# Performance work log

Measured on AMD Instinct MI355X. Metric: run time of the kernel, lower is better.

The kernel has to match this reference:

```python
import jax, jax.numpy as jnp
import numpy as np

N = 400_000      # active sparse voxels
C = 128          # hidden_size
GRID = 128       # dense grid extent per axis
KVOL = 27        # 3x3x3 kernel offsets


def _build_kmap():
    """Build a consistent neighbor map (the 'kmap') from random sparse voxel coords."""
    rng = np.random.default_rng(0)
    lin = np.sort(rng.choice(GRID ** 3, size=N, replace=False).astype(np.int64))
    lookup = np.full(GRID ** 3, -1, dtype=np.int32)
    lookup[lin] = np.arange(N, dtype=np.int32)
    x = lin // (GRID * GRID)
    y = (lin // GRID) % GRID
    z = lin % GRID
    nbr = np.full((N, KVOL), -1, dtype=np.int32)
    k = 0
    for dx in (-1, 0, 1):
        for dy in (-1, 0, 1):
            for dz in (-1, 0, 1):
                nx, ny, nz = x + dx, y + dy, z + dz
                valid = (nx >= 0) & (nx < GRID) & (ny >= 0) & (ny < GRID) & \
                        (nz >= 0) & (nz < GRID)
                nlin = (nx * GRID + ny) * GRID + nz
                nbr[:, k] = np.where(valid, lookup[np.clip(nlin, 0, GRID ** 3 - 1)], -1)
                k += 1
    return nbr


def setup_inputs() -> dict:
    key = jax.random.key(0)
    ks = jax.random.split(key, 6)
    s = 1.0 / np.sqrt(C)
    return {
        "feats": jax.random.normal(ks[0], (N, C), jnp.float32),
        "neighbor_idx": jnp.asarray(_build_kmap()),
        "conv_w": jax.random.normal(ks[1], (KVOL, C, C), jnp.float32) * (s / np.sqrt(KVOL)),
        "conv_b": jax.random.normal(ks[2], (C,), jnp.float32) * 0.01,
        "lin_w": jax.random.normal(ks[3], (C, C), jnp.float32) * s,   # torch Linear weight [out,in]
        "lin_b": jax.random.normal(ks[4], (C,), jnp.float32) * 0.01,
        "ln_g": jnp.ones((C,), jnp.float32),
        "ln_b": jnp.zeros((C,), jnp.float32),
    }


def reference(feats, neighbor_idx, conv_w, conv_b, lin_w, lin_b, ln_g, ln_b):
    # --- sparse 3x3x3 conv via kmap gather-GEMM-accumulate ---
    out = jnp.zeros_like(feats)
    for k in range(KVOL):  # fixed small structural loop over kernel offsets
        idx = neighbor_idx[:, k]
        valid = (idx >= 0)[:, None]
        gathered = jnp.where(valid, feats[jnp.maximum(idx, 0)], 0.0)  # [N, C]
        out = out + gathered @ conv_w[k]
    out = out + conv_b                      # conv bias add on jagged data
    # --- Linear (torch: x @ W.T + b) ---
    out = out @ lin_w.T + lin_b
    # --- LayerNorm over channel dim (eps=1e-5) ---
    mu = jnp.mean(out, axis=-1, keepdims=True)
    var = jnp.mean(jnp.square(out - mu), axis=-1, keepdims=True)
    out = (out - mu) * jax.lax.rsqrt(var + 1e-5) * ln_g + ln_b
    return out
```

## Files before the change

### kernel.cpp

```cpp
#include <hip/hip_runtime.h>

typedef __bf16 bf16;
typedef unsigned short u16;
typedef __attribute__((ext_vector_type(8))) __bf16 bf16x8;
typedef __attribute__((ext_vector_type(4))) float f32x4;
typedef const __attribute__((address_space(1))) char gchar;

#define N_PTS 400000
#define KVOL 27
#define SCHED0() __builtin_amdgcn_sched_barrier(0)

__device__ __forceinline__ f32x4 mfma16(bf16x8 a, bf16x8 b, f32x4 c) {
  return __builtin_amdgcn_mfma_f32_16x16x32_bf16(a, b, c, 0, 0, 0);
}

__global__ __launch_bounds__(256) void cast_feats_k(const float4* __restrict__ in,
                                                    bf16x8* __restrict__ out) {
  int i = blockIdx.x * 256 + threadIdx.x;
  float4 a = in[2 * i], b = in[2 * i + 1];
  bf16x8 v;
  v[0] = (bf16)a.x; v[1] = (bf16)a.y; v[2] = (bf16)a.z; v[3] = (bf16)a.w;
  v[4] = (bf16)b.x; v[5] = (bf16)b.y; v[6] = (bf16)b.z; v[7] = (bf16)b.w;
  out[i] = v;
}

__global__ __launch_bounds__(256) void cast_w_k(const float* __restrict__ conv_w,
                                                const float* __restrict__ lin_w,
                                                bf16x8* __restrict__ wt,
                                                bf16x8* __restrict__ lt,
                                                bf16x8* __restrict__ zrow) {
  int t = blockIdx.x * 256 + threadIdx.x;
  if (t < KVOL * 128 * 16) {
    int k = t >> 11;
    int rem = t & 2047;
    int co = rem >> 4;
    int cp = rem & 15;
    int cl = cp ^ (co & 7);
    bf16x8 v;
#pragma unroll
    for (int j = 0; j < 8; ++j) {
      int ci = cl * 8 + j;
      v[j] = (bf16)conv_w[(k * 128 + ci) * 128 + co];
    }
    wt[t] = v;
  } else if (t < KVOL * 128 * 16 + 2048) {
    int t2 = t - KVOL * 128 * 16;
    bf16x8 v;
#pragma unroll
    for (int j = 0; j < 8; ++j) v[j] = (bf16)lin_w[t2 * 8 + j];
    lt[t2] = v;
  } else if (t < KVOL * 128 * 16 + 2048 + 16) {
    bf16x8 v = {};
    zrow[t - (KVOL * 128 * 16 + 2048)] = v;
  }
}

__global__ __launch_bounds__(256, 2) void fused_k(
    const bf16* __restrict__ featsb,
    const int* __restrict__ nbr,
    const bf16* __restrict__ wt,
    const bf16* __restrict__ lt,
    const bf16* __restrict__ zrow,
    const float* __restrict__ conv_b,
    const float* __restrict__ lin_b,
    const float* __restrict__ ln_g,
    const float* __restrict__ ln_b,
    float* __restrict__ out) {
  __shared__ __align__(16) u16 wdb[2][16384];

  const int tid = threadIdx.x;
  const int lane = tid & 63;
  const int wv = tid >> 6;
  const int l15 = lane & 15;
  const int l4 = lane >> 4;
  const int lp = lane & 7;

  const int nwg = gridDim.x;
  const int bid0 = blockIdx.x;
  const int q = nwg >> 3, r8 = nwg & 7;
  const int xcd = bid0 & 7, lo = bid0 >> 3;
  const int bid = (xcd < r8 ? xcd * (q + 1) : r8 * (q + 1) + (xcd - r8) * q) + lo;

  const int row0 = bid * 256;
  const int rb = row0 + wv * 64 + l15;
  const int aoff = l4 * 16;

  {
    const char* g = (const char*)wt + (size_t)tid * 16;
    char* l = (char*)(&wdb[0][0]) + wv * 1024;
#pragma unroll
    for (int c = 0; c < 8; ++c)
      __builtin_amdgcn_global_load_lds(
          (const __attribute__((address_space(1))) void*)(g + c * 4096),
          (__attribute__((address_space(3))) void*)(l + c * 4096), 16, 0, 0);
  }
  int idx_nxt[4];
  int idx_t0[4];
#pragma unroll
  for (int rg = 0; rg < 4; ++rg) {
    int r = rb + rg * 16;
    int rr = r < N_PTS ? r : N_PTS - 1;
    int v0 = nbr[(size_t)rr * KVOL + 0];
    int v1 = nbr[(size_t)rr * KVOL + 1];
    idx_t0[rg] = r < N_PTS ? v0 : -1;
    idx_nxt[rg] = r < N_PTS ? v1 : -1;
  }
  bf16x8 a[4][4];
#pragma unroll
  for (int rg = 0; rg < 4; ++rg) {
    gchar* base = (idx_t0[rg] < 0)
                      ? (gchar*)zrow
                      : (gchar*)featsb + (size_t)idx_t0[rg] * 256;
    base += aoff;
#pragma unroll
    for (int kf = 0; kf < 4; ++kf) a[rg][kf] = *(const __attribute__((address_space(1))) bf16x8*)(base + kf * 64);
  }
  f32x4 acc[4][8];
#pragma unroll
  for (int rg = 0; rg < 4; ++rg)
#pragma unroll
    for (int ct = 0; ct < 8; ++ct) acc[rg][ct] = (f32x4)0.f;

  SCHED0();
  asm volatile("s_waitcnt vmcnt(0)" ::: "memory");
  SCHED0();
  __builtin_amdgcn_s_barrier();
  SCHED0();

  int cur = 0;
  for (int t = 0; t < KVOL; ++t) {
    {
      int tn = t + 1 < KVOL ? t + 1 : KVOL - 1;
      const char* g = (const char*)wt + (size_t)tn * 32768 + (size_t)tid * 16;
      char* l = (char*)(&wdb[cur ^ 1][0]) + wv * 1024;
#pragma unroll
      for (int c = 0; c < 8; ++c)
        __builtin_amdgcn_global_load_lds(
            (const __attribute__((address_space(1))) void*)(g + c * 4096),
            (__attribute__((address_space(3))) void*)(l + c * 4096), 16, 0, 0);
    }
    gchar* nb[4];
#pragma unroll
    for (int rg = 0; rg < 4; ++rg) {
      gchar* base = (idx_nxt[rg] < 0)
                        ? (gchar*)zrow
                        : (gchar*)featsb + (size_t)idx_nxt[rg] * 256;
      nb[rg] = base + aoff;
    }
    {
      int k2 = t + 2 < KVOL ? t + 2 : KVOL - 1;
#pragma unroll
      for (int rg = 0; rg < 4; ++rg) {
        int r = rb + rg * 16;
        int rr = r < N_PTS ? r : N_PTS - 1;
        int v = nbr[(size_t)rr * KVOL + k2];
        idx_nxt[rg] = r < N_PTS ? v : -1;
      }
    }
    SCHED0();
    asm volatile("s_waitcnt vmcnt(32)" ::: "memory");
    SCHED0();
    __builtin_amdgcn_s_barrier();
    SCHED0();
    const u16* wb = &wdb[cur][0];
#pragma unroll
    for (int kf = 0; kf < 4; ++kf) {
      const int chunk = (kf * 4 + l4) ^ lp;
      const u16* bp = wb + l15 * 128 + chunk * 8;
#pragma unroll
      for (int ct = 0; ct < 8; ++ct) {
        bf16x8 b = *(const bf16x8*)(bp + ct * 2048);
#pragma unroll
        for (int rg = 0; rg < 4; ++rg)
          acc[rg][ct] = mfma16(a[rg][kf], b, acc[rg][ct]);
      }
#pragma unroll
      for (int rg = 0; rg < 4; ++rg)
        a[rg][kf] = *(const __attribute__((address_space(1))) bf16x8*)(nb[rg] + kf * 64);
    }
    SCHED0();
    __builtin_amdgcn_s_barrier();
    SCHED0();
    cur ^= 1;
  }

  SCHED0();
  asm volatile("s_waitcnt vmcnt(0)" ::: "memory");
  SCHED0();
  __builtin_amdgcn_s_barrier();
  SCHED0();

  u16* cobuf = &wdb[0][0];
  float cb[8];
#pragma unroll
  for (int ct = 0; ct < 8; ++ct) cb[ct] = conv_b[ct * 16 + l15];
#pragma unroll
  for (int rg = 0; rg < 4; ++rg) {
#pragma unroll
    for (int ct = 0; ct < 8; ++ct) {
#pragma unroll
      for (int j = 0; j < 4; ++j) {
        int rl = wv * 64 + rg * 16 + l4 * 4 + j;
        int c = ct * 16 + l15;
        float x = acc[rg][ct][j] + cb[ct];
        int chunk = (c >> 3) ^ (rl & 7);
        cobuf[rl * 128 + chunk * 8 + (c & 7)] = __builtin_bit_cast(u16, (bf16)x);
      }
    }
  }
  SCHED0();
  asm volatile("s_waitcnt lgkmcnt(0)" ::: "memory");
  SCHED0();
  __builtin_amdgcn_s_barrier();
  SCHED0();

  f32x4 acc2[4][8];
#pragma unroll
  for (int rg = 0; rg < 4; ++rg)
#pragma unroll
    for (int ct = 0; ct < 8; ++ct) acc2[rg][ct] = (f32x4)0.f;
#pragma unroll
  for (int kf = 0; kf < 4; ++kf) {
    const int chunk = (kf * 4 + l4) ^ lp;
    bf16x8 av[4];
#pragma unroll
    for (int rg = 0; rg < 4; ++rg)
      av[rg] = *(const bf16x8*)(cobuf + (wv * 64 + rg * 16 + l15) * 128 + chunk * 8);
#pragma unroll
    for (int ct = 0; ct < 8; ++ct) {
      bf16x8 b = *(const bf16x8*)(lt + (ct * 16 + l15) * 128 + (kf * 4 + l4) * 8);
#pragma unroll
      for (int rg = 0; rg < 4; ++rg)
        acc2[rg][ct] = mfma16(av[rg], b, acc2[rg][ct]);
    }
  }

  float lb[8], lg[8], lbv[8];
#pragma unroll
  for (int ct = 0; ct < 8; ++ct) {
    int c = ct * 16 + l15;
    lb[ct] = lin_b[c]; lg[ct] = ln_g[c]; lbv[ct] = ln_b[c];
  }
#pragma unroll
  for (int rg = 0; rg < 4; ++rg) {
#pragma unroll
    for (int j = 0; j < 4; ++j) {
      float s = 0.f, qq = 0.f;
#pragma unroll
      for (int ct = 0; ct < 8; ++ct) {
        float x = acc2[rg][ct][j] + lb[ct];
        s += x; qq += x * x;
      }
#pragma unroll
      for (int m = 1; m <= 8; m <<= 1) {
        s += __shfl_xor(s, m, 64);
        qq += __shfl_xor(qq, m, 64);
      }
      float mu = s * (1.f / 128.f);
      float var = qq * (1.f / 128.f) - mu * mu;
      float rstd = rsqrtf(var + 1e-5f);
      int r = row0 + wv * 64 + rg * 16 + l4 * 4 + j;
      if (r < N_PTS) {
#pragma unroll
        for (int ct = 0; ct < 8; ++ct) {
          float x = acc2[rg][ct][j] + lb[ct];
          out[(size_t)r * 128 + ct * 16 + l15] = (x - mu) * rstd * lg[ct] + lbv[ct];
        }
      }
    }
  }
}

extern "C" void kernel_launch(void* const* d_in, const int* in_sizes, int n_in,
                              void* d_out, int out_size, void* d_ws, size_t ws_size,
                              hipStream_t stream) {
  const float* feats  = (const float*)d_in[0];
  const int*   nbr    = (const int*)d_in[1];
  const float* conv_w = (const float*)d_in[2];
  const float* conv_b = (const float*)d_in[3];
  const float* lin_w  = (const float*)d_in[4];
  const float* lin_b  = (const float*)d_in[5];
  const float* ln_g   = (const float*)d_in[6];
  const float* ln_b   = (const float*)d_in[7];
  float* out = (float*)d_out;

  bf16* featsb = (bf16*)d_ws;
  bf16* wt = featsb + (size_t)N_PTS * 128;
  bf16* lt = wt + (size_t)KVOL * 128 * 128;
  bf16* zrow = lt + (size_t)128 * 128;

  cast_feats_k<<<25000, 256, 0, stream>>>((const float4*)feats, (bf16x8*)featsb);
  cast_w_k<<<225, 256, 0, stream>>>(conv_w, lin_w, (bf16x8*)wt, (bf16x8*)lt, (bf16x8*)zrow);
  fused_k<<<1563, 256, 0, stream>>>(featsb, nbr, wt, lt, zrow,
                                    conv_b, lin_b, ln_g, ln_b, out);
}
```

Baseline: 434.2 us.

## Load conv weights directly from global in MFMA fragment layout, drop LDS staging

The weight-cast kernel now writes conv and linear weights pre-arranged in per-lane MFMA B-fragment order. The fused kernel then reads each B fragment with one coalesced 16-byte global load per lane (served from L2/cache), instead of double-buffering weight tiles through LDS. This removes the per-offset barriers and waitcnt synchronisation of the LDS pipeline, and s_setprio is raised around the MFMA bursts. The cost is more global/L2 traffic per wave, since every wave fetches the weights itself, and less explicit latency hiding.

```diff
diff --git a/kernel.cpp b/kernel.cpp
--- a/kernel.cpp
+++ b/kernel.cpp
@@ -5,6 +5,7 @@
 typedef __attribute__((ext_vector_type(8))) __bf16 bf16x8;
 typedef __attribute__((ext_vector_type(4))) float f32x4;
 typedef const __attribute__((address_space(1))) char gchar;
+typedef const __attribute__((address_space(1))) bf16x8 gbf16x8;
 
 #define N_PTS 400000
 #define KVOL 27
@@ -26,47 +27,51 @@
 
 __global__ __launch_bounds__(256) void cast_w_k(const float* __restrict__ conv_w,
                                                 const float* __restrict__ lin_w,
-                                                bf16x8* __restrict__ wt,
-                                                bf16x8* __restrict__ lt,
+                                                bf16x8* __restrict__ wt2,
+                                                bf16x8* __restrict__ lt2,
                                                 bf16x8* __restrict__ zrow) {
   int t = blockIdx.x * 256 + threadIdx.x;
-  if (t < KVOL * 128 * 16) {
+  if (t < KVOL * 4 * 8 * 64) {
+    int lane = t & 63;
+    int ct = (t >> 6) & 7;
+    int kf = (t >> 9) & 3;
     int k = t >> 11;
-    int rem = t & 2047;
-    int co = rem >> 4;
-    int cp = rem & 15;
-    int cl = cp ^ (co & 7);
+    int co = ct * 16 + (lane & 15);
+    int ci0 = kf * 32 + ((lane >> 4) & 3) * 8;
     bf16x8 v;
 #pragma unroll
-    for (int j = 0; j < 8; ++j) {
-      int ci = cl * 8 + j;
-      v[j] = (bf16)conv_w[(k * 128 + ci) * 128 + co];
-    }
-    wt[t] = v;
-  } else if (t < KVOL * 128 * 16 + 2048) {
-    int t2 = t - KVOL * 128 * 16;
+    for (int j = 0; j < 8; ++j)
+      v[j] = (bf16)conv_w[(k * 128 + ci0 + j) * 128 + co];
+    wt2[t] = v;
+  } else if (t < KVOL * 4 * 8 * 64 + 2048) {
+    int t2 = t - KVOL * 4 * 8 * 64;
+    int lane = t2 & 63;
+    int ct = (t2 >> 6) & 7;
+    int kf = t2 >> 9;
+    int co = ct * 16 + (lane & 15);
+    int ci0 = kf * 32 + ((lane >> 4) & 3) * 8;
     bf16x8 v;
 #pragma unroll
-    for (int j = 0; j < 8; ++j) v[j] = (bf16)lin_w[t2 * 8 + j];
-    lt[t2] = v;
-  } else if (t < KVOL * 128 * 16 + 2048 + 16) {
+    for (int j = 0; j < 8; ++j) v[j] = (bf16)lin_w[co * 128 + ci0 + j];
+    lt2[t2] = v;
+  } else if (t < KVOL * 4 * 8 * 64 + 2048 + 16) {
     bf16x8 v = {};
-    zrow[t - (KVOL * 128 * 16 + 2048)] = v;
+    zrow[t - (KVOL * 4 * 8 * 64 + 2048)] = v;
   }
 }
 
 __global__ __launch_bounds__(256, 2) void fused_k(
     const bf16* __restrict__ featsb,
     const int* __restrict__ nbr,
-    const bf16* __restrict__ wt,
-    const bf16* __restrict__ lt,
+    const bf16* __restrict__ wt2,
+    const bf16* __restrict__ lt2,
     const bf16* __restrict__ zrow,
     const float* __restrict__ conv_b,
     const float* __restrict__ lin_b,
     const float* __restrict__ ln_g,
     const float* __restrict__ ln_b,
     float* __restrict__ out) {
-  __shared__ __align__(16) u16 wdb[2][16384];
+  __shared__ __align__(16) u16 cobuf[256 * 128];
 
   const int tid = threadIdx.x;
   const int lane = tid & 63;
@@ -85,15 +90,6 @@
   const int rb = row0 + wv * 64 + l15;
   const int aoff = l4 * 16;
 
-  {
-    const char* g = (const char*)wt + (size_t)tid * 16;
-    char* l = (char*)(&wdb[0][0]) + wv * 1024;
-#pragma unroll
-    for (int c = 0; c < 8; ++c)
-      __builtin_amdgcn_global_load_lds(
-          (const __attribute__((address_space(1))) void*)(g + c * 4096),
-          (__attribute__((address_space(3))) void*)(l + c * 4096), 16, 0, 0);
-  }
   int idx_nxt[4];
   int idx_t0[4];
 #pragma unroll
@@ -108,12 +104,11 @@
   bf16x8 a[4][4];
 #pragma unroll
   for (int rg = 0; rg < 4; ++rg) {
-    gchar* base = (idx_t0[rg] < 0)
-                      ? (gchar*)zrow
-                      : (gchar*)featsb + (size_t)idx_t0[rg] * 256;
+    gchar* base = (idx_t0[rg] < 0) ? (gchar*)zrow
+                                   : (gchar*)featsb + (size_t)idx_t0[rg] * 256;
     base += aoff;
 #pragma unroll
-    for (int kf = 0; kf < 4; ++kf) a[rg][kf] = *(const __attribute__((address_space(1))) bf16x8*)(base + kf * 64);
+    for (int kf = 0; kf < 4; ++kf) a[rg][kf] = *(gbf16x8*)(base + kf * 64);
   }
   f32x4 acc[4][8];
 #pragma unroll
@@ -121,30 +116,12 @@
 #pragma unroll
     for (int ct = 0; ct < 8; ++ct) acc[rg][ct] = (f32x4)0.f;
 
-  SCHED0();
-  asm volatile("s_waitcnt vmcnt(0)" ::: "memory");
-  SCHED0();
-  __builtin_amdgcn_s_barrier();
-  SCHED0();
-
-  int cur = 0;
   for (int t = 0; t < KVOL; ++t) {
-    {
-      int tn = t + 1 < KVOL ? t + 1 : KVOL - 1;
-      const char* g = (const char*)wt + (size_t)tn * 32768 + (size_t)tid * 16;
-      char* l = (char*)(&wdb[cur ^ 1][0]) + wv * 1024;
-#pragma unroll
-      for (int c = 0; c < 8; ++c)
-        __builtin_amdgcn_global_load_lds(
-            (const __attribute__((address_space(1))) void*)(g + c * 4096),
-            (__attribute__((address_space(3))) void*)(l + c * 4096), 16, 0, 0);
-    }
     gchar* nb[4];
 #pragma unroll
     for (int rg = 0; rg < 4; ++rg) {
-      gchar* base = (idx_nxt[rg] < 0)
-                        ? (gchar*)zrow
-                        : (gchar*)featsb + (size_t)idx_nxt[rg] * 256;
+      gchar* base = (idx_nxt[rg] < 0) ? (gchar*)zrow
+                                      : (gchar*)featsb + (size_t)idx_nxt[rg] * 256;
       nb[rg] = base + aoff;
     }
     {
@@ -157,40 +134,25 @@
         idx_nxt[rg] = r < N_PTS ? v : -1;
       }
     }
-    SCHED0();
-    asm volatile("s_waitcnt vmcnt(32)" ::: "memory");
-    SCHED0();
-    __builtin_amdgcn_s_barrier();
-    SCHED0();
-    const u16* wb = &wdb[cur][0];
+    gchar* wb = (gchar*)wt2 + (size_t)t * 32768 + (size_t)lane * 16;
 #pragma unroll
     for (int kf = 0; kf < 4; ++kf) {
-      const int chunk = (kf * 4 + l4) ^ lp;
-      const u16* bp = wb + l15 * 128 + chunk * 8;
-#pragma unroll
-      for (int ct = 0; ct < 8; ++ct) {
-        bf16x8 b = *(const bf16x8*)(bp + ct * 2048);
+      bf16x8 b[8];
+#pragma unroll
+      for (int ct = 0; ct < 8; ++ct)
+        b[ct] = *(gbf16x8*)(wb + kf * 8192 + ct * 1024);
+      __builtin_amdgcn_s_setprio(1);
+#pragma unroll
+      for (int ct = 0; ct < 8; ++ct)
 #pragma unroll
         for (int rg = 0; rg < 4; ++rg)
-          acc[rg][ct] = mfma16(a[rg][kf], b, acc[rg][ct]);
-      }
-#pragma unroll
-      for (int rg = 0; rg < 4; ++rg)
-        a[rg][kf] = *(const __attribute__((address_space(1))) bf16x8*)(nb[rg] + kf * 64);
-    }
-    SCHED0();
-    __builtin_amdgcn_s_barrier();
-    SCHED0();
-    cur ^= 1;
-  }
-
-  SCHED0();
-  asm volatile("s_waitcnt vmcnt(0)" ::: "memory");
-  SCHED0();
-  __builtin_amdgcn_s_barrier();
-  SCHED0();
-
-  u16* cobuf = &wdb[0][0];
+          acc[rg][ct] = mfma16(a[rg][kf], b[ct], acc[rg][ct]);
+      __builtin_amdgcn_s_setprio(0);
+#pragma unroll
+      for (int rg = 0; rg < 4; ++rg) a[rg][kf] = *(gbf16x8*)(nb[rg] + kf * 64);
+    }
+  }
+
   float cb[8];
 #pragma unroll
   for (int ct = 0; ct < 8; ++ct) cb[ct] = conv_b[ct * 16 + l15];
@@ -208,11 +170,7 @@
       }
     }
   }
-  SCHED0();
-  asm volatile("s_waitcnt lgkmcnt(0)" ::: "memory");
-  SCHED0();
-  __builtin_amdgcn_s_barrier();
-  SCHED0();
+  __syncthreads();
 
   f32x4 acc2[4][8];
 #pragma unroll
@@ -228,7 +186,7 @@
       av[rg] = *(const bf16x8*)(cobuf + (wv * 64 + rg * 16 + l15) * 128 + chunk * 8);
 #pragma unroll
     for (int ct = 0; ct < 8; ++ct) {
-      bf16x8 b = *(const bf16x8*)(lt + (ct * 16 + l15) * 128 + (kf * 4 + l4) * 8);
+      bf16x8 b = *(gbf16x8*)((gchar*)lt2 + (kf * 8 + ct) * 1024 + lane * 16);
 #pragma unroll
       for (int rg = 0; rg < 4; ++rg)
         acc2[rg][ct] = mfma16(av[rg], b, acc2[rg][ct]);
@@ -285,12 +243,12 @@
   float* out = (float*)d_out;
 
   bf16* featsb = (bf16*)d_ws;
-  bf16* wt = featsb + (size_t)N_PTS * 128;
-  bf16* lt = wt + (size_t)KVOL * 128 * 128;
-  bf16* zrow = lt + (size_t)128 * 128;
+  bf16* wt2 = featsb + (size_t)N_PTS * 128;
+  bf16* lt2 = wt2 + (size_t)KVOL * 128 * 128;
+  bf16* zrow = lt2 + (size_t)128 * 128;
 
   cast_feats_k<<<25000, 256, 0, stream>>>((const float4*)feats, (bf16x8*)featsb);
-  cast_w_k<<<225, 256, 0, stream>>>(conv_w, lin_w, (bf16x8*)wt, (bf16x8*)lt, (bf16x8*)zrow);
-  fused_k<<<1563, 256, 0, stream>>>(featsb, nbr, wt, lt, zrow,
+  cast_w_k<<<225, 256, 0, stream>>>(conv_w, lin_w, (bf16x8*)wt2, (bf16x8*)lt2, (bf16x8*)zrow);
+  fused_k<<<1563, 256, 0, stream>>>(featsb, nbr, wt2, lt2, zrow,
                                     conv_b, lin_b, ln_g, ln_b, out);
 }
```

After: 617.8 us. 42.3% more time.
